# Kernel optimization log

Measured on AMD Instinct MI355X. Metric: run time of the kernel, lower is better.

## Reference

```python
import jax, jax.numpy as jnp
import numpy as np

D_MODEL = 1024
N_HEADS = 16
D_HEAD = 64
SCALE = D_HEAD ** -0.5


def setup_inputs() -> dict:
    key = jax.random.key(0)
    k1, k2, k3, k4, k5 = jax.random.split(key, 5)
    B, N = 8, 1024
    x = jax.random.normal(k1, (B, N, D_MODEL), dtype=jnp.float32)
    qkv_w = jax.random.normal(k2, (3 * D_MODEL, D_MODEL), dtype=jnp.float32) * (D_MODEL ** -0.5)
    qkv_b = jax.random.normal(k3, (3 * D_MODEL,), dtype=jnp.float32) * 0.02
    proj_w = jax.random.normal(k4, (D_MODEL, D_MODEL), dtype=jnp.float32) * (D_MODEL ** -0.5)
    proj_b = jax.random.normal(k5, (D_MODEL,), dtype=jnp.float32) * 0.02
    return {"x": x, "qkv_w": qkv_w, "qkv_b": qkv_b, "proj_w": proj_w, "proj_b": proj_b}


def reference(x, qkv_w, qkv_b, proj_w, proj_b):
    B, N, C = x.shape
    # qkv projection (torch Linear: x @ W.T + b)
    qkv = x @ qkv_w.T + qkv_b                      # [B, N, 3*C]
    qkv = qkv.reshape(B, N, 3, N_HEADS, D_HEAD)
    qkv = jnp.transpose(qkv, (2, 0, 3, 1, 4))      # [3, B, H, N, d]
    q, k, v = qkv[0], qkv[1], qkv[2]
    q = q * SCALE
    attn_scores = jnp.einsum('bhqd,bhkd->bhqk', q, k)   # [B, H, N, N]
    attn_pattern = jax.nn.softmax(attn_scores, axis=-1)
    attn_pattern = jnp.where(jnp.isnan(attn_pattern), jnp.zeros_like(attn_pattern), attn_pattern)
    z = jnp.einsum('bhqk,bhkd->bhqd', attn_pattern, v)   # [B, H, N, d]
    z = jnp.transpose(z, (0, 2, 1, 3)).reshape(B, N, C)
    return z @ proj_w.T + proj_b
```

## Files before the change

kernel.cpp:

```cpp
#include <hip/hip_runtime.h>
#include <hip/hip_fp16.h>

typedef _Float16 half8 __attribute__((ext_vector_type(8)));
typedef _Float16 half4v __attribute__((ext_vector_type(4)));
typedef float f32x4 __attribute__((ext_vector_type(4)));

#define GAS1(p) ((const __attribute__((address_space(1))) void*)(p))
#define LAS3(p) ((__attribute__((address_space(3))) void*)(p))

#define SCALE 0.125f
#define LOG2E 1.44269504088896340736f
#define RESCALE_THR 8.0f

__global__ void cvt_all(const float* __restrict__ x, const float* __restrict__ qw,
                        const float* __restrict__ pw, _Float16* __restrict__ xb,
                        _Float16* __restrict__ wqkv, _Float16* __restrict__ wproj) {
  const int b = blockIdx.x;
  const float* src;
  _Float16* dst;
  int j;
  if (b < 8192)       { src = x;  dst = xb;    j = b * 256 + threadIdx.x; }
  else if (b < 11264) { src = qw; dst = wqkv;  j = (b - 8192) * 256 + threadIdx.x; }
  else                { src = pw; dst = wproj; j = (b - 11264) * 256 + threadIdx.x; }
  float4 f = reinterpret_cast<const float4*>(src)[j];
  half4v h;
  h[0] = (_Float16)f.x; h[1] = (_Float16)f.y;
  h[2] = (_Float16)f.z; h[3] = (_Float16)f.w;
  reinterpret_cast<half4v*>(dst)[j] = h;
}

template<int EPI>
__launch_bounds__(512, 1)
__global__ void gemm256(const _Float16* __restrict__ A, const _Float16* __restrict__ Bw,
                        const float* __restrict__ bias, float* __restrict__ Cf,
                        _Float16* __restrict__ qo, _Float16* __restrict__ ko,
                        _Float16* __restrict__ vto, int Kdim, int Ndim) {
  __shared__ alignas(128) _Float16 lds[2][2][2][128 * 64];
  const int tid = threadIdx.x;
  const int w = tid >> 6, lane = tid & 63, lo = lane & 15, hi = lane >> 4;
  const int wm = w >> 2, wn = w & 3;
  const int tm0 = blockIdx.x * 256, tn0 = blockIdx.y * 256;
  const int T = Kdim >> 6;

  auto stage = [&](int op, int t, int half) {
    const _Float16* src = (op ? Bw + (size_t)(tn0 + half * 128) * Kdim
                              : A + (size_t)(tm0 + half * 128) * Kdim) + t * 64;
    char* dst = (char*)&lds[t & 1][op][half][0] + w * 1024;
#pragma unroll
    for (int qq = 0; qq < 2; ++qq) {
      int o = qq * 8192 + w * 1024 + lane * 16;
      int row = o >> 7;
      int kk = ((o & 127) ^ ((row & 7) << 4)) >> 1;
      __builtin_amdgcn_global_load_lds(GAS1(src + (size_t)row * Kdim + kk),
                                       LAS3(dst + qq * 8192), 16, 0, 0);
    }
  };

  f32x4 acc[8][4] = {};

  stage(0, 0, 0); stage(0, 0, 1); stage(1, 0, 0); stage(1, 0, 1);
  stage(1, 1, 0); stage(1, 1, 1);
  asm volatile("s_waitcnt vmcnt(0)" ::: "memory");
  __builtin_amdgcn_sched_barrier(0);
  __builtin_amdgcn_s_barrier();
  __builtin_amdgcn_sched_barrier(0);

  for (int t = 0; t < T; ++t) {
    const char* Ab = (const char*)&lds[t & 1][0][wm][0];
    const char* Bb = (const char*)&lds[t & 1][1][wn >> 1][0];
    const int nrow0 = (wn & 1) * 64;
    half8 af[4][2], bf[4][2];

#pragma unroll
    for (int m = 0; m < 4; ++m) {
      int row = m * 16 + lo;
#pragma unroll
      for (int s = 0; s < 2; ++s)
        af[m][s] = *reinterpret_cast<const half8*>(
            Ab + (row << 7) + ((s * 64 + hi * 16) ^ ((row & 7) << 4)));
    }
#pragma unroll
    for (int n = 0; n < 2; ++n) {
      int row = nrow0 + n * 16 + lo;
#pragma unroll
      for (int s = 0; s < 2; ++s)
        bf[n][s] = *reinterpret_cast<const half8*>(
            Bb + (row << 7) + ((s * 64 + hi * 16) ^ ((row & 7) << 4)));
    }
    if (t + 1 < T) stage(0, t + 1, 0);
    __builtin_amdgcn_sched_barrier(0);
    __builtin_amdgcn_s_barrier();
    __builtin_amdgcn_sched_barrier(0);
    __builtin_amdgcn_s_setprio(1);
#pragma unroll
    for (int m = 0; m < 4; ++m)
#pragma unroll
      for (int n = 0; n < 2; ++n)
#pragma unroll
        for (int s = 0; s < 2; ++s)
          acc[m][n] = __builtin_amdgcn_mfma_f32_16x16x32_f16(af[m][s], bf[n][s], acc[m][n], 0, 0, 0);
    __builtin_amdgcn_s_setprio(0);

#pragma unroll
    for (int n = 2; n < 4; ++n) {
      int row = nrow0 + n * 16 + lo;
#pragma unroll
      for (int s = 0; s < 2; ++s)
        bf[n][s] = *reinterpret_cast<const half8*>(
            Bb + (row << 7) + ((s * 64 + hi * 16) ^ ((row & 7) << 4)));
    }
    if (t + 1 < T) stage(0, t + 1, 1);
    __builtin_amdgcn_sched_barrier(0);
    __builtin_amdgcn_s_barrier();
    __builtin_amdgcn_sched_barrier(0);
    __builtin_amdgcn_s_setprio(1);
#pragma unroll
    for (int m = 0; m < 4; ++m)
#pragma unroll
      for (int n = 2; n < 4; ++n)
#pragma unroll
        for (int s = 0; s < 2; ++s)
          acc[m][n] = __builtin_amdgcn_mfma_f32_16x16x32_f16(af[m][s], bf[n][s], acc[m][n], 0, 0, 0);
    __builtin_amdgcn_s_setprio(0);

#pragma unroll
    for (int m = 0; m < 4; ++m) {
      int row = 64 + m * 16 + lo;
#pragma unroll
      for (int s = 0; s < 2; ++s)
        af[m][s] = *reinterpret_cast<const half8*>(
            Ab + (row << 7) + ((s * 64 + hi * 16) ^ ((row & 7) << 4)));
    }
    if (t + 2 < T) { stage(1, t + 2, 0); stage(1, t + 2, 1); }
    __builtin_amdgcn_sched_barrier(0);
    __builtin_amdgcn_s_barrier();
    __builtin_amdgcn_sched_barrier(0);
    __builtin_amdgcn_s_setprio(1);
#pragma unroll
    for (int m = 0; m < 4; ++m)
#pragma unroll
      for (int n = 0; n < 4; ++n)
#pragma unroll
        for (int s = 0; s < 2; ++s)
          acc[4 + m][n] = __builtin_amdgcn_mfma_f32_16x16x32_f16(af[m][s], bf[n][s], acc[4 + m][n], 0, 0, 0);
    __builtin_amdgcn_s_setprio(0);

    if (t + 1 < T) {
      if (t + 2 < T) asm volatile("s_waitcnt vmcnt(4)" ::: "memory");
      else           asm volatile("s_waitcnt vmcnt(0)" ::: "memory");
      __builtin_amdgcn_sched_barrier(0);
      __builtin_amdgcn_s_barrier();
      __builtin_amdgcn_sched_barrier(0);
    }
  }

  if (EPI == 0) {
#pragma unroll
    for (int M = 0; M < 8; ++M) {
      const int gm = tm0 + wm * 128 + M * 16 + hi * 4;
#pragma unroll
      for (int n = 0; n < 4; ++n) {
        const int gc = tn0 + wn * 64 + n * 16 + lo;
        const float bj = bias[gc];
#pragma unroll
        for (int u = 0; u < 4; ++u)
          Cf[(size_t)(gm + u) * Ndim + gc] = acc[M][n][u] + bj;
      }
    }
  } else {
    const int tsel = tn0 >> 10;
#pragma unroll
    for (int M = 0; M < 8; ++M) {
      const int gm = tm0 + wm * 128 + M * 16 + hi * 4;
      const int b = gm >> 10;
      const int nr = gm & 1023;
#pragma unroll
      for (int n = 0; n < 4; ++n) {
        const int gc = tn0 + wn * 64 + n * 16 + lo;
        const float bj = bias[gc];
        const int h = (gc >> 6) & 15;
        const int d = gc & 63;
        const size_t hb = ((size_t)(b * 16 + h)) << 16;
        if (tsel == 0) {
#pragma unroll
          for (int u = 0; u < 4; ++u)
            qo[hb + (size_t)(nr + u) * 64 + d] = (_Float16)((acc[M][n][u] + bj) * SCALE);
        } else if (tsel == 1) {
#pragma unroll
          for (int u = 0; u < 4; ++u)
            ko[hb + (size_t)(nr + u) * 64 + d] = (_Float16)(acc[M][n][u] + bj);
        } else {
          half4v v4;
#pragma unroll
          for (int u = 0; u < 4; ++u) v4[u] = (_Float16)(acc[M][n][u] + bj);
          *reinterpret_cast<half4v*>(vto + hb + (size_t)d * 1024 + nr) = v4;
        }
      }
    }
  }
}

__launch_bounds__(256, 4)
__global__ void attn_kernel(const _Float16* __restrict__ q, const _Float16* __restrict__ kb,
                            const _Float16* __restrict__ vt, _Float16* __restrict__ z) {
  __shared__ alignas(128) _Float16 Ks[2][64 * 64];
  __shared__ alignas(128) _Float16 Vs[2][64 * 64];
  __shared__ alignas(128) _Float16 P[4][16 * 64];
  const int tid = threadIdx.x;
  const int w = tid >> 6, lane = tid & 63, lo = lane & 15, hi = lane >> 4;
  const int bh = blockIdx.y;
  const int qr0 = blockIdx.x * 128 + w * 32;
  const size_t base = (size_t)bh << 16;

  auto stage = [&](int buf, int kt) {
#pragma unroll
    for (int p = 0; p < 2; ++p) {
      int o = p * 4096 + w * 1024 + lane * 16;
      int row = o >> 7;
      int kk = ((o & 127) ^ ((row & 7) << 4)) >> 1;
      __builtin_amdgcn_global_load_lds(GAS1(kb + base + (size_t)(kt + row) * 64 + kk),
                                       LAS3((char*)&Ks[buf][0] + p * 4096 + w * 1024), 16, 0, 0);
      __builtin_amdgcn_global_load_lds(GAS1(vt + base + (size_t)row * 1024 + kt + kk),
                                       LAS3((char*)&Vs[buf][0] + p * 4096 + w * 1024), 16, 0, 0);
    }
  };

  stage(0, 0);

  half8 qf[2][2];
#pragma unroll
  for (int rg = 0; rg < 2; ++rg)
#pragma unroll
    for (int s = 0; s < 2; ++s)
      qf[rg][s] = *reinterpret_cast<const half8*>(
          q + base + (size_t)(qr0 + rg * 16 + lo) * 64 + s * 32 + hi * 8);

  f32x4 zacc[2][4] = {};
  float m_s[2] = {-1e30f, -1e30f};
  float l_s[2] = {0.f, 0.f};

  char* Pw = (char*)&P[w][0];
  __syncthreads();

  int buf = 0;
  for (int kt = 0; kt < 1024; kt += 64) {
    if (kt + 64 < 1024) stage(buf ^ 1, kt + 64);
    const char* Kb = (const char*)&Ks[buf][0];
    const char* Vb = (const char*)&Vs[buf][0];

    f32x4 sacc[2][4];
#pragma unroll
    for (int rg = 0; rg < 2; ++rg)
#pragma unroll
      for (int c = 0; c < 4; ++c) sacc[rg][c] = f32x4{0.f, 0.f, 0.f, 0.f};
#pragma unroll
    for (int c = 0; c < 4; ++c) {
      const int row = c * 16 + lo;
      half8 bK0 = *reinterpret_cast<const half8*>(
          Kb + (row << 7) + ((hi * 16) ^ ((row & 7) << 4)));
      half8 bK1 = *reinterpret_cast<const half8*>(
          Kb + (row << 7) + ((64 + hi * 16) ^ ((row & 7) << 4)));
      __builtin_amdgcn_s_setprio(1);
#pragma unroll
      for (int rg = 0; rg < 2; ++rg) {
        sacc[rg][c] = __builtin_amdgcn_mfma_f32_16x16x32_f16(bK0, qf[rg][0], sacc[rg][c], 0, 0, 0);
        sacc[rg][c] = __builtin_amdgcn_mfma_f32_16x16x32_f16(bK1, qf[rg][1], sacc[rg][c], 0, 0, 0);
      }
      __builtin_amdgcn_s_setprio(0);
    }

#pragma unroll
    for (int rg = 0; rg < 2; ++rg) {
      float tmax = fmaxf(
          fmaxf(fmaxf(fmaxf(sacc[rg][0][0], sacc[rg][0][1]), fmaxf(sacc[rg][0][2], sacc[rg][0][3])),
                fmaxf(fmaxf(sacc[rg][1][0], sacc[rg][1][1]), fmaxf(sacc[rg][1][2], sacc[rg][1][3]))),
          fmaxf(fmaxf(fmaxf(sacc[rg][2][0], sacc[rg][2][1]), fmaxf(sacc[rg][2][2], sacc[rg][2][3])),
                fmaxf(fmaxf(sacc[rg][3][0], sacc[rg][3][1]), fmaxf(sacc[rg][3][2], sacc[rg][3][3]))));
      if (!__all(tmax <= m_s[rg] + RESCALE_THR)) {
        float t2 = fmaxf(tmax, __shfl_xor(tmax, 16));
        t2 = fmaxf(t2, __shfl_xor(t2, 32));
        float mn = fmaxf(m_s[rg], t2);
        float alpha = exp2f((m_s[rg] - mn) * LOG2E);
        m_s[rg] = mn;
        l_s[rg] *= alpha;
#pragma unroll
        for (int v = 0; v < 4; ++v)
#pragma unroll
          for (int u = 0; u < 4; ++u) zacc[rg][v][u] *= alpha;
      }
      const float ml = m_s[rg] * LOG2E;
      float psum = 0.f;
#pragma unroll
      for (int c = 0; c < 4; ++c)
#pragma unroll
        for (int u = 0; u < 4; ++u) {
          float p = exp2f(sacc[rg][c][u] * LOG2E - ml);
          sacc[rg][c][u] = p;
          psum += p;
        }
      l_s[rg] += psum;

#pragma unroll
      for (int c = 0; c < 4; ++c) {
        half4v p4;
#pragma unroll
        for (int u = 0; u < 4; ++u) p4[u] = (_Float16)sacc[rg][c][u];
        int byteoff = (lo << 7) + ((c * 32 + hi * 8) ^ ((lo & 7) << 4));
        *reinterpret_cast<half4v*>(Pw + byteoff) = p4;
      }

#pragma unroll
      for (int s = 0; s < 2; ++s) {
        int pbyte = (lo << 7) + ((hi * 16 + s * 64) ^ ((lo & 7) << 4));
        half8 pf = *reinterpret_cast<const half8*>((const char*)Pw + pbyte);
        half8 bV[4];
#pragma unroll
        for (int v = 0; v < 4; ++v) {
          int row = v * 16 + lo;
          bV[v] = *reinterpret_cast<const half8*>(
              Vb + (row << 7) + ((s * 64 + hi * 16) ^ ((row & 7) << 4)));
        }
        __builtin_amdgcn_s_setprio(1);
#pragma unroll
        for (int v = 0; v < 4; ++v)
          zacc[rg][v] = __builtin_amdgcn_mfma_f32_16x16x32_f16(bV[v], pf, zacc[rg][v], 0, 0, 0);
        __builtin_amdgcn_s_setprio(0);
      }
    }
    __syncthreads();
    buf ^= 1;
  }

  const int b = bh >> 4, h = bh & 15;
#pragma unroll
  for (int rg = 0; rg < 2; ++rg) {
    float l = l_s[rg];
    l += __shfl_xor(l, 16);
    l += __shfl_xor(l, 32);
    const float rl = 1.0f / l;
    const int qrow = qr0 + rg * 16 + lo;
#pragma unroll
    for (int v = 0; v < 4; ++v) {
      half4v o;
#pragma unroll
      for (int u = 0; u < 4; ++u) o[u] = (_Float16)(zacc[rg][v][u] * rl);
      *reinterpret_cast<half4v*>(
          z + ((size_t)b * 1024 + qrow) * 1024 + h * 64 + v * 16 + hi * 4) = o;
    }
  }
}

extern "C" void kernel_launch(void* const* d_in, const int* in_sizes, int n_in,
                              void* d_out, int out_size, void* d_ws, size_t ws_size,
                              hipStream_t stream) {
  const float* x      = (const float*)d_in[0];
  const float* qkv_w  = (const float*)d_in[1];
  const float* qkv_b  = (const float*)d_in[2];
  const float* proj_w = (const float*)d_in[3];
  const float* proj_b = (const float*)d_in[4];
  float* out = (float*)d_out;

  _Float16* ws    = (_Float16*)d_ws;
  _Float16* xb    = ws;
  _Float16* wqkv  = ws + 8388608;
  _Float16* wproj = ws + 11534336;
  _Float16* qb    = ws + 12582912;
  _Float16* kbb   = ws + 20971520;
  _Float16* vtb   = ws + 29360128;
  _Float16* zb    = ws + 37748736;

  cvt_all<<<12288, 256, 0, stream>>>(x, qkv_w, proj_w, xb, wqkv, wproj);

  gemm256<1><<<dim3(32, 12), 512, 0, stream>>>(xb, wqkv, qkv_b, nullptr,
                                               qb, kbb, vtb, 1024, 3072);
  attn_kernel<<<dim3(8, 128), 256, 0, stream>>>(qb, kbb, vtb, zb);
  gemm256<0><<<dim3(32, 4), 512, 0, stream>>>(zb, wproj, proj_b, out,
                                              nullptr, nullptr, nullptr, 1024, 1024);
}
```

Measured before the change: 262.2 us.

## Use smaller-tile GEMM for output projection and MFMA-based softmax row sums

The output projection moves from the 256-tile GEMM (128 blocks) to a new 128x128-tile GEMM with 512 blocks, so more CUs have work, at the cost of less reuse per tile and no double buffering. Separately, the attention kernel stops summing softmax probabilities with scalar adds and cross-lane shuffles. It instead adds an extra MFMA against a vector of ones, reading the same fp16 P that feeds the PV product. This trades VALU work for one more matrix instruction per step and makes the normalizer use fp16-rounded probabilities.

```diff
diff --git a/kernel.cpp b/kernel.cpp
--- a/kernel.cpp
+++ b/kernel.cpp
@@ -200,6 +200,67 @@
   }
 }
 
+__launch_bounds__(256, 2)
+__global__ void gemm128(const _Float16* __restrict__ A, const _Float16* __restrict__ Bw,
+                        const float* __restrict__ bias, float* __restrict__ Cf,
+                        int Kdim, int Ndim) {
+  __shared__ alignas(128) _Float16 As[128 * 64];
+  __shared__ alignas(128) _Float16 Bs[128 * 64];
+  const int tid = threadIdx.x;
+  const int w = tid >> 6, lane = tid & 63, lo = lane & 15, hi = lane >> 4;
+  const int wr = w >> 1, wc = w & 1;
+  const int tm0 = blockIdx.x * 128;
+  const int tn0 = blockIdx.y * 128;
+
+  f32x4 acc[4][4] = {};
+
+  for (int k0 = 0; k0 < Kdim; k0 += 64) {
+    __syncthreads();
+#pragma unroll
+    for (int r = 0; r < 4; ++r) {
+      int o = r * 4096 + w * 1024 + lane * 16;
+      int row = o >> 7;
+      int kk = ((o & 127) ^ ((row & 7) << 4)) >> 1;
+      __builtin_amdgcn_global_load_lds(GAS1(A + (size_t)(tm0 + row) * Kdim + k0 + kk),
+                                       LAS3((char*)As + r * 4096 + w * 1024), 16, 0, 0);
+      __builtin_amdgcn_global_load_lds(GAS1(Bw + (size_t)(tn0 + row) * Kdim + k0 + kk),
+                                       LAS3((char*)Bs + r * 4096 + w * 1024), 16, 0, 0);
+    }
+    __syncthreads();
+#pragma unroll
+    for (int s = 0; s < 2; ++s) {
+      half8 af[4], bf[4];
+#pragma unroll
+      for (int i = 0; i < 4; ++i) {
+        int arow = wr * 64 + i * 16 + lo;
+        int abyte = (arow << 7) + ((hi * 16 + s * 64) ^ ((arow & 7) << 4));
+        af[i] = *reinterpret_cast<const half8*>((const char*)As + abyte);
+        int brow = wc * 64 + i * 16 + lo;
+        int bbyte = (brow << 7) + ((hi * 16 + s * 64) ^ ((brow & 7) << 4));
+        bf[i] = *reinterpret_cast<const half8*>((const char*)Bs + bbyte);
+      }
+#pragma unroll
+      for (int i = 0; i < 4; ++i)
+#pragma unroll
+        for (int j = 0; j < 4; ++j)
+          acc[i][j] = __builtin_amdgcn_mfma_f32_16x16x32_f16(af[i], bf[j], acc[i][j], 0, 0, 0);
+    }
+  }
+
+#pragma unroll
+  for (int i = 0; i < 4; ++i) {
+    const int m0 = tm0 + wr * 64 + i * 16 + hi * 4;
+#pragma unroll
+    for (int j = 0; j < 4; ++j) {
+      const int n = tn0 + wc * 64 + j * 16 + lo;
+      const float bj = bias[n];
+#pragma unroll
+      for (int r = 0; r < 4; ++r)
+        Cf[(size_t)(m0 + r) * Ndim + n] = acc[i][j][r] + bj;
+    }
+  }
+}
+
 __launch_bounds__(256, 4)
 __global__ void attn_kernel(const _Float16* __restrict__ q, const _Float16* __restrict__ kb,
                             const _Float16* __restrict__ vt, _Float16* __restrict__ z) {
@@ -235,9 +296,13 @@
       qf[rg][s] = *reinterpret_cast<const half8*>(
           q + base + (size_t)(qr0 + rg * 16 + lo) * 64 + s * 32 + hi * 8);
 
+  half8 ones;
+#pragma unroll
+  for (int j = 0; j < 8; ++j) ones[j] = (_Float16)1.0f;
+
   f32x4 zacc[2][4] = {};
+  f32x4 zsum[2] = {};
   float m_s[2] = {-1e30f, -1e30f};
-  float l_s[2] = {0.f, 0.f};
 
   char* Pw = (char*)&P[w][0];
   __syncthreads();
@@ -282,23 +347,19 @@
         float mn = fmaxf(m_s[rg], t2);
         float alpha = exp2f((m_s[rg] - mn) * LOG2E);
         m_s[rg] = mn;
-        l_s[rg] *= alpha;
+#pragma unroll
+        for (int u = 0; u < 4; ++u) zsum[rg][u] *= alpha;
 #pragma unroll
         for (int v = 0; v < 4; ++v)
 #pragma unroll
           for (int u = 0; u < 4; ++u) zacc[rg][v][u] *= alpha;
       }
       const float ml = m_s[rg] * LOG2E;
-      float psum = 0.f;
 #pragma unroll
       for (int c = 0; c < 4; ++c)
 #pragma unroll
-        for (int u = 0; u < 4; ++u) {
-          float p = exp2f(sacc[rg][c][u] * LOG2E - ml);
-          sacc[rg][c][u] = p;
-          psum += p;
-        }
-      l_s[rg] += psum;
+        for (int u = 0; u < 4; ++u)
+          sacc[rg][c][u] = exp2f(sacc[rg][c][u] * LOG2E - ml);
 
 #pragma unroll
       for (int c = 0; c < 4; ++c) {
@@ -321,6 +382,7 @@
               Vb + (row << 7) + ((s * 64 + hi * 16) ^ ((row & 7) << 4)));
         }
         __builtin_amdgcn_s_setprio(1);
+        zsum[rg] = __builtin_amdgcn_mfma_f32_16x16x32_f16(ones, pf, zsum[rg], 0, 0, 0);
 #pragma unroll
         for (int v = 0; v < 4; ++v)
           zacc[rg][v] = __builtin_amdgcn_mfma_f32_16x16x32_f16(bV[v], pf, zacc[rg][v], 0, 0, 0);
@@ -334,10 +396,7 @@
   const int b = bh >> 4, h = bh & 15;
 #pragma unroll
   for (int rg = 0; rg < 2; ++rg) {
-    float l = l_s[rg];
-    l += __shfl_xor(l, 16);
-    l += __shfl_xor(l, 32);
-    const float rl = 1.0f / l;
+    const float rl = 1.0f / zsum[rg][0];
     const int qrow = qr0 + rg * 16 + lo;
 #pragma unroll
     for (int v = 0; v < 4; ++v) {
@@ -374,6 +433,5 @@
   gemm256<1><<<dim3(32, 12), 512, 0, stream>>>(xb, wqkv, qkv_b, nullptr,
                                                qb, kbb, vtb, 1024, 3072);
   attn_kernel<<<dim3(8, 128), 256, 0, stream>>>(qb, kbb, vtb, zb);
-  gemm256<0><<<dim3(32, 4), 512, 0, stream>>>(zb, wproj, proj_b, out,
-                                              nullptr, nullptr, nullptr, 1024, 1024);
+  gemm128<<<dim3(64, 8), 256, 0, stream>>>(zb, wproj, proj_b, out, 1024, 1024);
 }
```

After: 255.0 us. -2.7%, faster.
